# Optimization experiments

Measured on AMD Instinct MI355X. Metric: run time of the kernel, lower is better.

Reference implementation:

```python
import jax, jax.numpy as jnp
import numpy as np

B, N, DS, DP, H, DH, DFF = 1, 1024, 768, 128, 16, 48, 1536


def _ln(x, eps=1e-5):
    m = jnp.mean(x, axis=-1, keepdims=True)
    v = jnp.var(x, axis=-1, keepdims=True)
    return (x - m) * jax.lax.rsqrt(v + eps)


def _ada_ln(a, s, gw, gb, bw):
    # AF3-style adaptive layernorm: sigmoid(Linear(LN(s))) * LN(a) + Linear(LN(s))
    sn = _ln(s)
    return jax.nn.sigmoid(sn @ gw + gb) * _ln(a) + sn @ bw


def setup_inputs() -> dict:
    key = jax.random.key(0)
    ks = jax.random.split(key, 24)
    w = lambda k, shape: jax.random.normal(k, shape, dtype=jnp.float32) * 0.02
    return {
        'x': jax.random.normal(ks[0], (B, N, DS), dtype=jnp.float32),
        'single_cond': jax.random.normal(ks[1], (B, N, DS), dtype=jnp.float32),
        'pair_cond': jax.random.normal(ks[2], (B, N, N, DP), dtype=jnp.float32),
        'attn_gamma_w': w(ks[3], (DS, DS)), 'attn_gamma_b': jnp.zeros((DS,), jnp.float32),
        'attn_beta_w': w(ks[4], (DS, DS)),
        'wq': w(ks[5], (DS, H * DH)), 'bq': jnp.zeros((H * DH,), jnp.float32),
        'wk': w(ks[6], (DS, H * DH)), 'wv': w(ks[7], (DS, H * DH)),
        'wb': w(ks[8], (DP, H)),
        'wg': w(ks[9], (DS, H * DH)),
        'wo': w(ks[10], (H * DH, DS)),
        'attn_gate_w': w(ks[11], (DS, DS)), 'attn_gate_b': jnp.full((DS,), -2.0, jnp.float32),
        'ff_gamma_w': w(ks[12], (DS, DS)), 'ff_gamma_b': jnp.zeros((DS,), jnp.float32),
        'ff_beta_w': w(ks[13], (DS, DS)),
        'ff_w1': w(ks[14], (DS, DFF)), 'ff_w2': w(ks[15], (DS, DFF)),
        'ff_w3': w(ks[16], (DFF, DS)),
        'ff_gate_w': w(ks[17], (DS, DS)), 'ff_gate_b': jnp.full((DS,), -2.0, jnp.float32),
        'mask': jnp.ones((B, N), dtype=bool),
    }


def reference(x, single_cond, pair_cond, attn_gamma_w, attn_gamma_b, attn_beta_w,
              wq, bq, wk, wv, wb, wg, wo, attn_gate_w, attn_gate_b,
              ff_gamma_w, ff_gamma_b, ff_beta_w, ff_w1, ff_w2, ff_w3,
              ff_gate_w, ff_gate_b, mask):
    # --- AttentionPairBias (edge bias + cond adaLN + gated output) ---
    a = _ada_ln(x, single_cond, attn_gamma_w, attn_gamma_b, attn_beta_w)
    q = (a @ wq + bq).reshape(B, N, H, DH)  # q has bias (q_use_bias=True)
    k = (a @ wk).reshape(B, N, H, DH)
    v = (a @ wv).reshape(B, N, H, DH)
    bias = jnp.einsum('bijp,ph->bhij', _ln(pair_cond), wb)  # pair bias per head
    logits = jnp.einsum('bihd,bjhd->bhij', q, k) * (1.0 / np.float32(np.sqrt(DH))) + bias
    logits = jnp.where(mask[:, None, None, :], logits, jnp.float32(-1e9))
    attn = jax.nn.softmax(logits, axis=-1)
    o = jnp.einsum('bhij,bjhd->bihd', attn, v)
    g = jax.nn.sigmoid(a @ wg).reshape(B, N, H, DH)  # gating (g_use_bias=False)
    attn_out = (g * o).reshape(B, N, H * DH) @ wo  # o_use_bias=False
    attn_out = jax.nn.sigmoid(single_cond @ attn_gate_w + attn_gate_b) * attn_out
    # --- ConditionedFeedForward (adaLN + SwiGLU + cond output gate) ---
    f = _ada_ln(x, single_cond, ff_gamma_w, ff_gamma_b, ff_beta_w)
    h = jax.nn.silu(f @ ff_w1) * (f @ ff_w2)
    ff_out = jax.nn.sigmoid(single_cond @ ff_gate_w + ff_gate_b) * (h @ ff_w3)
    # dropout p=0 (eval) -> identity; residual add of both branches
    return x + attn_out + ff_out
```

## Files before the change

kernel.cpp:

```cpp
#include <hip/hip_runtime.h>
#include <hip/hip_bf16.h>


typedef __attribute__((ext_vector_type(8))) short bf16x8;
typedef __attribute__((ext_vector_type(4))) float f32x4;
typedef __attribute__((ext_vector_type(4))) unsigned short us4;

#define DEVFN static __device__ __forceinline__

DEVFN float bf2f(unsigned short u){
  union { unsigned int u; float f; } v; v.u = ((unsigned int)u) << 16; return v.f;
}
DEVFN unsigned short f2bf(float f){
  union { float f; unsigned int u; } v; v.f = f;
  unsigned int r = v.u + 0x7fffu + ((v.u >> 16) & 1u);
  return (unsigned short)(r >> 16);
}
DEVFN float sigf(float x){ return 1.f / (1.f + __expf(-x)); }

DEVFN void gload16(const void* g, void* l){
  __builtin_amdgcn_global_load_lds(
      (const __attribute__((address_space(1))) void*)g,
      (__attribute__((address_space(3))) void*)l, 16, 0, 0);
}

#define OFF_SN    0x0000000ULL
#define OFF_SC    0x0180000ULL
#define OFF_XA    0x0300000ULL
#define OFF_W1    0x0600000ULL
#define OFF_W2    0x0A80000ULL
#define OFF_W3    0x0CC0000ULL
#define OFF_W4    0x1140000ULL
#define OFF_W5    0x15C0000ULL
#define OFF_W6    0x1800000ULL
#define OFF_BIAS1 0x1920000ULL
#define OFF_BIASG 0x1923000ULL
#define OFF_BIASQ 0x1924800ULL
#define OFF_G1    0x1930000ULL
#define OFF_GATES 0x2530000ULL
#define OFF_A     0x2B30000ULL
#define OFF_F     0x2CB0000ULL
#define OFF_QKVG  0x2E30000ULL
#define OFF_VT    0x3430000ULL
#define OFF_HH    0x4030000ULL
#define OFF_GO    0x4330000ULL
#define OFF_PB    0x47B0000ULL

struct WJobs {
  const float* src[14];
  unsigned long long dst[14];
  int K[14];
  int N[14];
  int rowmul[14];
  int rowoff[14];
};

__global__ __launch_bounds__(256) void prep_kernel(WJobs jobs, char* ws,
    const float* __restrict__ x, const float* __restrict__ sc,
    unsigned short* __restrict__ sn_bf, unsigned short* __restrict__ sc_bf,
    float* __restrict__ xa,
    const float* agb, const float* bq, const float* gtb, const float* fgtb,
    const float* fgb, float* bias1, float* biasg, float* biasq){
  const int bid = blockIdx.x;
  const int tid = threadIdx.x;
  if(bid < 9792){
    int t = bid, z = 0;
    while(true){
      int nt = (jobs.N[z] >> 5) * (jobs.K[z] >> 5);
      if(t < nt) break;
      t -= nt; z++;
    }
    const int nx = jobs.N[z] >> 5;
    const int n0 = (t % nx) << 5, k0 = (t / nx) << 5;
    const int K = jobs.K[z], N = jobs.N[z];
    __shared__ float tt[32][33];
    const int tx = tid & 31, ty = tid >> 5;
    const float* src = jobs.src[z];
    #pragma unroll
    for(int i=0;i<4;i++)
      tt[ty + i*8][tx] = src[(long long)(k0 + ty + i*8) * N + n0 + tx];
    __syncthreads();
    unsigned short* dst = (unsigned short*)(ws + jobs.dst[z]);
    const int rm = jobs.rowmul[z], ro = jobs.rowoff[z];
    #pragma unroll
    for(int i=0;i<4;i++)
      dst[(long long)((n0 + ty + i*8)*rm + ro) * K + k0 + tx] = f2bf(tt[tx][ty + i*8]);
    return;
  }
  if(bid >= 10816){
    int t = (bid - 10816) * 256 + tid;
    float v = 0.f;
    if(t < 768) v = agb[t];
    else if(t >= 1536 && t < 2304) v = fgb[t - 1536];
    bias1[t] = v;
    biasq[t] = (t < 768) ? bq[t] : 0.f;
    if(t < 1536) biasg[t] = (t < 768) ? gtb[t] : fgtb[t - 768];
    return;
  }
  const int row = bid - 9792;
  const float* xr = x + (long long)row * 768;
  const float* sr = sc + (long long)row * 768;
  float xs[3], ss[3];
  float s0=0.f, s1=0.f, s2=0.f, s3=0.f;
  #pragma unroll
  for(int i=0;i<3;i++){
    float xv = xr[tid + i*256], sv = sr[tid + i*256];
    xs[i]=xv; ss[i]=sv;
    s0 += xv; s1 += xv*xv; s2 += sv; s3 += sv*sv;
  }
  #pragma unroll
  for(int o=32;o;o>>=1){
    s0 += __shfl_xor(s0,o); s1 += __shfl_xor(s1,o);
    s2 += __shfl_xor(s2,o); s3 += __shfl_xor(s3,o);
  }
  __shared__ float red[4][4];
  const int w = tid >> 6;
  if((tid & 63) == 0){ red[0][w]=s0; red[1][w]=s1; red[2][w]=s2; red[3][w]=s3; }
  __syncthreads();
  float tx0 = red[0][0]+red[0][1]+red[0][2]+red[0][3];
  float tx1 = red[1][0]+red[1][1]+red[1][2]+red[1][3];
  float ts0 = red[2][0]+red[2][1]+red[2][2]+red[2][3];
  float ts1 = red[3][0]+red[3][1]+red[3][2]+red[3][3];
  const float inv = 1.f/768.f;
  float mx = tx0*inv, vx = tx1*inv - mx*mx;
  float ms = ts0*inv, vs = ts1*inv - ms*ms;
  float rsx = rsqrtf(vx + 1e-5f), rss = rsqrtf(vs + 1e-5f);
  #pragma unroll
  for(int i=0;i<3;i++){
    int c = tid + i*256;
    xa[(long long)row*768 + c]    = (xs[i]-mx)*rsx;
    sn_bf[(long long)row*768 + c] = f2bf((ss[i]-ms)*rss);
    sc_bf[(long long)row*768 + c] = f2bf(ss[i]);
  }
}

DEVFN void gemm_tile_f32(const unsigned short* __restrict__ A,
                         const unsigned short* __restrict__ Bt,
                         int N, int K, int m0, int n0,
                         const float* __restrict__ bias,
                         float* __restrict__ Cf, int epi,
                         unsigned short* sA, unsigned short* sB, int tid){
  const int w = tid >> 6, l = tid & 63, l15 = l & 15, l4 = l >> 4;
  const int wm = w >> 1, wn = w & 1;
  f32x4 zf = {0.f,0.f,0.f,0.f};
  f32x4 acc[4][4];
  #pragma unroll
  for(int m=0;m<4;m++)
    #pragma unroll
    for(int n=0;n<4;n++) acc[m][n] = zf;

  const int srow = w*16 + (l >> 2);
  const int scol = (l & 3) * 8;
  const unsigned short* gA = A  + (long long)(m0 + srow) * K + scol;
  const unsigned short* gB = Bt + (long long)(n0 + srow) * K + scol;
  unsigned short* lA0 = &sA[(w*16)*32];
  unsigned short* lA1 = &sA[(64 + w*16)*32];
  unsigned short* lB0 = &sB[(w*16)*32];
  unsigned short* lB1 = &sB[(64 + w*16)*32];
  const long long half = (long long)64 * K;

  for(int k0 = 0; k0 < K; k0 += 32){
    gload16(gA + k0, lA0);
    gload16(gA + half + k0, lA1);
    gload16(gB + k0, lB0);
    gload16(gB + half + k0, lB1);
    __syncthreads();
    bf16x8 af[4], bg[4];
    #pragma unroll
    for(int m=0;m<4;m++) af[m] = *(const bf16x8*)&sA[(wm*64 + m*16 + l15)*32 + l4*8];
    #pragma unroll
    for(int n=0;n<4;n++) bg[n] = *(const bf16x8*)&sB[(wn*64 + n*16 + l15)*32 + l4*8];
    #pragma unroll
    for(int m=0;m<4;m++)
      #pragma unroll
      for(int n=0;n<4;n++)
        acc[m][n] = __builtin_amdgcn_mfma_f32_16x16x32_bf16(af[m], bg[n], acc[m][n], 0, 0, 0);
    __syncthreads();
  }
  #pragma unroll
  for(int m=0;m<4;m++){
    #pragma unroll
    for(int n=0;n<4;n++){
      #pragma unroll
      for(int r=0;r<4;r++){
        const int i = m0 + wm*64 + m*16 + l4*4 + r;
        const int c = n0 + wn*64 + n*16 + l15;
        float v = acc[m][n][r] + bias[c];
        Cf[(long long)i*N + c] = epi ? sigf(v) : v;
      }
    }
  }
}

DEVFN void pair_block(int pbid, const float* __restrict__ pair,
                      const float* __restrict__ wb,
                      unsigned short* __restrict__ pb, int tid){
  const int l = tid & 63, w = tid >> 6, l15 = l & 15, l4 = l >> 4;
  bf16x8 wbf[4];
  #pragma unroll
  for(int c=0;c<4;c++){
    bf16x8 t;
    #pragma unroll
    for(int e=0;e<8;e++) t[e] = (short)f2bf(wb[(c*32 + l4*8 + e)*16 + l15]);
    wbf[c] = t;
  }
  f32x4 zf = {0.f,0.f,0.f,0.f};
  #pragma unroll
  for(int q=0;q<4;q++){
    const long long tile = (long long)pbid * 16 + q*4 + w;
    const long long row0 = tile << 4;
    const float* pr = pair + ((row0 + l15) << 7);
    float vals[32];
    #pragma unroll
    for(int c=0;c<4;c++){
      float4 v0 = *(const float4*)(pr + c*32 + l4*8);
      float4 v1 = *(const float4*)(pr + c*32 + l4*8 + 4);
      vals[c*8+0]=v0.x; vals[c*8+1]=v0.y; vals[c*8+2]=v0.z; vals[c*8+3]=v0.w;
      vals[c*8+4]=v1.x; vals[c*8+5]=v1.y; vals[c*8+6]=v1.z; vals[c*8+7]=v1.w;
    }
    float s=0.f, s2=0.f;
    #pragma unroll
    for(int e=0;e<32;e++){ s += vals[e]; s2 += vals[e]*vals[e]; }
    s += __shfl_xor(s, 16); s2 += __shfl_xor(s2, 16);
    s += __shfl_xor(s, 32); s2 += __shfl_xor(s2, 32);
    const float m = s * (1.f/128.f);
    const float rs = rsqrtf(s2*(1.f/128.f) - m*m + 1e-5f);
    f32x4 acc = zf;
    #pragma unroll
    for(int c=0;c<4;c++){
      bf16x8 af;
      #pragma unroll
      for(int e=0;e<8;e++) af[e] = (short)f2bf((vals[c*8+e] - m) * rs);
      acc = __builtin_amdgcn_mfma_f32_16x16x32_bf16(af, wbf[c], acc, 0,0,0);
    }
    us4 o;
    #pragma unroll
    for(int r=0;r<4;r++) o[r] = f2bf(acc[r]);
    *(us4*)&pb[((long long)l15 << 20) + row0 + l4*4] = o;
  }
}

__global__ __launch_bounds__(256) void fA_kernel(
    const float* __restrict__ pair, const float* __restrict__ wb,
    unsigned short* __restrict__ pb,
    const unsigned short* __restrict__ SN, const unsigned short* __restrict__ W1,
    const float* __restrict__ B1, float* __restrict__ G1,
    const unsigned short* __restrict__ SC, const unsigned short* __restrict__ W2,
    const float* __restrict__ BG, float* __restrict__ GT){
  __shared__ unsigned short sA[128*32];
  __shared__ unsigned short sB[128*32];
  const int bid = blockIdx.x;
  const int tid = threadIdx.x;
  if(bid < 288){
    if(bid < 192){
      gemm_tile_f32(SN, W1, 3072, 768, (bid & 7)*128, (bid >> 3)*128, B1, G1, 0, sA, sB, tid);
    } else {
      const int t = bid - 192;
      gemm_tile_f32(SC, W2, 1536, 768, (t & 7)*128, (t >> 3)*128, BG, GT, 1, sA, sB, tid);
    }
    return;
  }
  pair_block(bid - 288, pair, wb, pb, tid);
}

__global__ __launch_bounds__(256) void ew1_kernel(const float* __restrict__ g1,
    const float* __restrict__ xa, unsigned short* __restrict__ a_bf,
    unsigned short* __restrict__ f_bf, const float* __restrict__ x,
    float* __restrict__ out){
  const int i = blockIdx.x;
  const int c = blockIdx.y * 256 + threadIdx.x;
  const float* row = g1 + (long long)i * 3072;
  float xv = xa[(long long)i*768 + c];
  a_bf[(long long)i*768 + c] = f2bf(sigf(row[c])      * xv + row[768 + c]);
  f_bf[(long long)i*768 + c] = f2bf(sigf(row[1536+c]) * xv + row[2304 + c]);
  out[(long long)i*768 + c] = x[(long long)i*768 + c];
}

__global__ __launch_bounds__(256) void fB_kernel(
    const float* __restrict__ pair, const float* __restrict__ wb,
    unsigned short* __restrict__ pb,
    const unsigned short* __restrict__ A_, const unsigned short* __restrict__ W3,
    const float* __restrict__ BQ, unsigned short* __restrict__ QKVG,
    unsigned short* __restrict__ VT,
    const unsigned short* __restrict__ F_, const unsigned short* __restrict__ W4,
    unsigned short* __restrict__ HH){
  __shared__ unsigned short sA[128*32];
  __shared__ unsigned short sB[128*32];
  const int bid = blockIdx.x;
  const int tid = threadIdx.x;
  if(bid >= 384){
    pair_block(bid - 384 + 2048, pair, wb, pb, tid);
    return;
  }
  const bool isq = bid < 192;
  const int t = isq ? bid : bid - 192;
  const int m0 = (t & 7) * 128, n0 = (t >> 3) * 128;
  const unsigned short* A  = isq ? A_ : F_;
  const unsigned short* Bt = isq ? W3 : W4;
  const int K = 768;

  const int w = tid >> 6, l = tid & 63, l15 = l & 15, l4 = l >> 4;
  const int wm = w >> 1, wn = w & 1;
  f32x4 zf = {0.f,0.f,0.f,0.f};
  f32x4 acc[4][4];
  #pragma unroll
  for(int m=0;m<4;m++)
    #pragma unroll
    for(int n=0;n<4;n++) acc[m][n] = zf;

  const int srow = w*16 + (l >> 2);
  const int scol = (l & 3) * 8;
  const unsigned short* gA = A  + (long long)(m0 + srow) * K + scol;
  const unsigned short* gB = Bt + (long long)(n0 + srow) * K + scol;
  unsigned short* lA0 = &sA[(w*16)*32];
  unsigned short* lA1 = &sA[(64 + w*16)*32];
  unsigned short* lB0 = &sB[(w*16)*32];
  unsigned short* lB1 = &sB[(64 + w*16)*32];
  const long long half = (long long)64 * K;

  for(int k0 = 0; k0 < K; k0 += 32){
    gload16(gA + k0, lA0);
    gload16(gA + half + k0, lA1);
    gload16(gB + k0, lB0);
    gload16(gB + half + k0, lB1);
    __syncthreads();
    bf16x8 af[4], bg[4];
    #pragma unroll
    for(int m=0;m<4;m++) af[m] = *(const bf16x8*)&sA[(wm*64 + m*16 + l15)*32 + l4*8];
    #pragma unroll
    for(int n=0;n<4;n++) bg[n] = *(const bf16x8*)&sB[(wn*64 + n*16 + l15)*32 + l4*8];
    #pragma unroll
    for(int m=0;m<4;m++)
      #pragma unroll
      for(int n=0;n<4;n++)
        acc[m][n] = __builtin_amdgcn_mfma_f32_16x16x32_bf16(af[m], bg[n], acc[m][n], 0, 0, 0);
    __syncthreads();
  }
  if(isq){
    #pragma unroll
    for(int m=0;m<4;m++){
      #pragma unroll
      for(int n=0;n<4;n++){
        const int c = n0 + wn*64 + n*16 + l15;
        const int ibase = m0 + wm*64 + m*16 + l4*4;
        unsigned short vb[4];
        #pragma unroll
        for(int r=0;r<4;r++){
          vb[r] = f2bf(acc[m][n][r] + BQ[c]);
          QKVG[(long long)(ibase + r)*3072 + c] = vb[r];
        }
        if(c >= 1536 && c < 2304){
          us4 o; o.x=vb[0]; o.y=vb[1]; o.z=vb[2]; o.w=vb[3];
          *(us4*)&VT[((long long)(c - 1536) << 10) + ibase] = o;
        }
      }
    }
  } else {
    #pragma unroll
    for(int m=0;m<4;m++){
      #pragma unroll
      for(int n=0;n<4;n++){
        #pragma unroll
        for(int r=0;r<4;r++){
          const int i = m0 + wm*64 + m*16 + l4*4 + r;
          const int c = n0 + wn*64 + n*16 + l15;
          float v = acc[m][n][r];
          float partner = __shfl_xor(v, 1);
          if((c & 1) == 0)
            HH[(long long)i*1536 + (c>>1)] = f2bf(v * sigf(v) * partner);
        }
      }
    }
  }
}

__global__ __launch_bounds__(256) void attn_kernel(
    const unsigned short* __restrict__ qkvg,
    const unsigned short* __restrict__ pbias,
    const unsigned short* __restrict__ VT,
    unsigned short* __restrict__ go){
  const int h  = blockIdx.x >> 6;
  const int i0 = (blockIdx.x & 63) << 4;
  const int tid = threadIdx.x;
  const int w = tid >> 6, l = tid & 63, l15 = l & 15, l4 = l >> 4;

  __shared__ unsigned short sP[16][1032];
  __shared__ float sRedM[16][4];
  __shared__ float sRedS[16][4];
  __shared__ float sO[4][16][48];

  f32x4 zf = {0.f,0.f,0.f,0.f};
  bf16x8 zero8 = {0,0,0,0,0,0,0,0};

  const unsigned short* pbh = pbias + ((long long)h << 20) + ((long long)i0 << 10);
  #pragma unroll
  for(int it=0; it<8; it++){
    const int idx = it*2048 + tid*8;
    const int r = idx >> 10, c = idx & 1023;
    *(bf16x8*)&sP[r][c] = *(const bf16x8*)&pbh[((long long)r << 10) + c];
  }

  f32x4 accs[16];
  #pragma unroll
  for(int f=0;f<16;f++) accs[f] = zf;
  bf16x8 aq0, aq1;
  {
    const unsigned short* qp = qkvg + (long long)(i0 + l15)*3072 + h*48;
    aq0 = *(const bf16x8*)(qp + l4*8);
    aq1 = *(const bf16x8*)(qp + 32 + l4*8);
  }
  const int jbase = w * 256;
  #pragma unroll
  for(int f=0; f<16; f++){
    const int j = jbase + f*16 + l15;
    const unsigned short* kp = qkvg + (long long)j*3072 + 768 + h*48;
    bf16x8 bk0 = *(const bf16x8*)(kp + l4*8);
    bf16x8 bk1 = *(const bf16x8*)(kp + 32 + l4*8);
    if(l4 >= 2) bk1 = zero8;
    accs[f] = __builtin_amdgcn_mfma_f32_16x16x32_bf16(aq0, bk0, accs[f], 0,0,0);
    accs[f] = __builtin_amdgcn_mfma_f32_16x16x32_bf16(aq1, bk1, accs[f], 0,0,0);
  }
  __syncthreads();

  const float scale = 0.14433756729740643f;
  #pragma unroll
  for(int f=0;f<16;f++){
    #pragma unroll
    for(int r=0;r<4;r++)
      accs[f][r] = accs[f][r]*scale + bf2f(sP[l4*4 + r][jbase + f*16 + l15]);
  }
  float pm[4];
  #pragma unroll
  for(int r=0;r<4;r++){
    float m = accs[0][r];
    #pragma unroll
    for(int f=1;f<16;f++) m = fmaxf(m, accs[f][r]);
    #pragma unroll
    for(int o=1;o<16;o<<=1) m = fmaxf(m, __shfl_xor(m, o));
    pm[r] = m;
  }
  if(l15 == 0){
    #pragma unroll
    for(int r=0;r<4;r++) sRedM[l4*4 + r][w] = pm[r];
  }
  __syncthreads();
  float rowm[4];
  #pragma unroll
  for(int r=0;r<4;r++){
    const int i = l4*4 + r;
    rowm[r] = fmaxf(fmaxf(sRedM[i][0], sRedM[i][1]), fmaxf(sRedM[i][2], sRedM[i][3]));
  }
  float psum[4] = {0.f,0.f,0.f,0.f};
  #pragma unroll
  for(int f=0;f<16;f++)
    #pragma unroll
    for(int r=0;r<4;r++){
      float p = __expf(accs[f][r] - rowm[r]);
      accs[f][r] = p;
      psum[r] += p;
    }
  #pragma unroll
  for(int r=0;r<4;r++)
    #pragma unroll
    for(int o=1;o<16;o<<=1) psum[r] += __shfl_xor(psum[r], o);
  if(l15 == 0){
    #pragma unroll
    for(int r=0;r<4;r++) sRedS[l4*4 + r][w] = psum[r];
  }
  #pragma unroll
  for(int f=0;f<16;f++)
    #pragma unroll
    for(int r=0;r<4;r++)
      sP[l4*4 + r][jbase + f*16 + l15] = f2bf(accs[f][r]);

  f32x4 acco[3];
  #pragma unroll
  for(int n=0;n<3;n++) acco[n] = zf;
  const unsigned short* vth = VT + ((long long)(h*48) << 10);
  #pragma unroll
  for(int c=0; c<4; c++){
    const int jb = jbase + c*64;
    #pragma unroll
    for(int kk=0; kk<2; kk++){
      bf16x8 pa = *(const bf16x8*)&sP[l15][jb + kk*32 + l4*8];
      #pragma unroll
      for(int n=0;n<3;n++){
        bf16x8 bv = *(const bf16x8*)&vth[((long long)(n*16 + l15) << 10) + jb + kk*32 + l4*8];
        acco[n] = __builtin_amdgcn_mfma_f32_16x16x32_bf16(pa, bv, acco[n], 0,0,0);
      }
    }
  }
  #pragma unroll
  for(int n=0;n<3;n++)
    #pragma unroll
    for(int r=0;r<4;r++)
      sO[w][l4*4 + r][n*16 + l15] = acco[n][r];
  __syncthreads();
  for(int t = tid; t < 768; t += 256){
    const int i = t / 48, d = t % 48;
    float o = sO[0][i][d] + sO[1][i][d] + sO[2][i][d] + sO[3][i][d];
    float lsum = sRedS[i][0] + sRedS[i][1] + sRedS[i][2] + sRedS[i][3];
    float gv = bf2f(qkvg[(long long)(i0 + i)*3072 + 2304 + h*48 + d]);
    go[(long long)(i0 + i)*768 + h*48 + d] = f2bf(sigf(gv) * (o / lsum));
  }
}

__global__ __launch_bounds__(256) void final_kernel(
    const unsigned short* __restrict__ GO, const unsigned short* __restrict__ W6t,
    const unsigned short* __restrict__ HH, const unsigned short* __restrict__ W5t,
    const float* __restrict__ gates, float* __restrict__ out){
  __shared__ unsigned short sA[128*32];
  __shared__ unsigned short sB[128*32];
  const int m0 = blockIdx.x * 128, n0 = blockIdx.y * 128;
  const int z = blockIdx.z;
  const bool pA = z < 4;
  const unsigned short* A  = pA ? GO  : HH;
  const unsigned short* Bt = pA ? W6t : W5t;
  const int K    = pA ? 768 : 1536;
  const int kbeg = pA ? z*192 : (z-4)*384;
  const int kend = pA ? kbeg + 192 : kbeg + 384;
  const int goff = pA ? 0 : 768;
  const int tid = threadIdx.x;
  const int w = tid >> 6, l = tid & 63, l15 = l & 15, l4 = l >> 4;
  const int wm = w >> 1, wn = w & 1;
  f32x4 zf = {0.f,0.f,0.f,0.f};
  f32x4 acc[4][4];
  #pragma unroll
  for(int m=0;m<4;m++)
    #pragma unroll
    for(int n=0;n<4;n++) acc[m][n] = zf;

  const int srow = w*16 + (l >> 2);
  const int scol = (l & 3) * 8;
  const unsigned short* gA = A  + (long long)(m0 + srow) * K + scol;
  const unsigned short* gB = Bt + (long long)(n0 + srow) * K + scol;
  unsigned short* lA0 = &sA[(w*16)*32];
  unsigned short* lA1 = &sA[(64 + w*16)*32];
  unsigned short* lB0 = &sB[(w*16)*32];
  unsigned short* lB1 = &sB[(64 + w*16)*32];
  const long long half = (long long)64 * K;

  for(int k0 = kbeg; k0 < kend; k0 += 32){
    gload16(gA + k0, lA0);
    gload16(gA + half + k0, lA1);
    gload16(gB + k0, lB0);
    gload16(gB + half + k0, lB1);
    __syncthreads();
    bf16x8 af[4], bg[4];
    #pragma unroll
    for(int m=0;m<4;m++) af[m] = *(const bf16x8*)&sA[(wm*64 + m*16 + l15)*32 + l4*8];
    #pragma unroll
    for(int n=0;n<4;n++) bg[n] = *(const bf16x8*)&sB[(wn*64 + n*16 + l15)*32 + l4*8];
    #pragma unroll
    for(int m=0;m<4;m++)
      #pragma unroll
      for(int n=0;n<4;n++)
        acc[m][n] = __builtin_amdgcn_mfma_f32_16x16x32_bf16(af[m], bg[n], acc[m][n], 0, 0, 0);
    __syncthreads();
  }
  #pragma unroll
  for(int m=0;m<4;m++){
    #pragma unroll
    for(int n=0;n<4;n++){
      #pragma unroll
      for(int r=0;r<4;r++){
        const int i = m0 + wm*64 + m*16 + l4*4 + r;
        const int c = n0 + wn*64 + n*16 + l15;
        float v = gates[(long long)i*1536 + goff + c] * acc[m][n][r];
        __hip_atomic_fetch_add(&out[(long long)i*768 + c], v,
                               __ATOMIC_RELAXED, __HIP_MEMORY_SCOPE_AGENT);
      }
    }
  }
}

extern "C" void kernel_launch(void* const* d_in, const int* in_sizes, int n_in,
                              void* d_out, int out_size, void* d_ws, size_t ws_size,
                              hipStream_t stream){
  (void)in_sizes; (void)n_in; (void)out_size; (void)ws_size;
  const float* x    = (const float*)d_in[0];
  const float* sc   = (const float*)d_in[1];
  const float* pair = (const float*)d_in[2];
  const float* agw  = (const float*)d_in[3];
  const float* agb  = (const float*)d_in[4];
  const float* abw  = (const float*)d_in[5];
  const float* wq   = (const float*)d_in[6];
  const float* bq   = (const float*)d_in[7];
  const float* wk   = (const float*)d_in[8];
  const float* wv   = (const float*)d_in[9];
  const float* wb   = (const float*)d_in[10];
  const float* wg   = (const float*)d_in[11];
  const float* wo   = (const float*)d_in[12];
  const float* gtw  = (const float*)d_in[13];
  const float* gtb  = (const float*)d_in[14];
  const float* fgw  = (const float*)d_in[15];
  const float* fgb  = (const float*)d_in[16];
  const float* fbw  = (const float*)d_in[17];
  const float* fw1  = (const float*)d_in[18];
  const float* fw2  = (const float*)d_in[19];
  const float* fw3  = (const float*)d_in[20];
  const float* fgtw = (const float*)d_in[21];
  const float* fgtb = (const float*)d_in[22];
  float* out = (float*)d_out;
  char* ws = (char*)d_ws;

  unsigned short* SN   = (unsigned short*)(ws + OFF_SN);
  unsigned short* SC   = (unsigned short*)(ws + OFF_SC);
  float*          XA   = (float*)(ws + OFF_XA);
  unsigned short* W1   = (unsigned short*)(ws + OFF_W1);
  unsigned short* W2   = (unsigned short*)(ws + OFF_W2);
  unsigned short* W3   = (unsigned short*)(ws + OFF_W3);
  unsigned short* W4   = (unsigned short*)(ws + OFF_W4);
  unsigned short* W5   = (unsigned short*)(ws + OFF_W5);
  unsigned short* W6   = (unsigned short*)(ws + OFF_W6);
  float*          B1   = (float*)(ws + OFF_BIAS1);
  float*          BG   = (float*)(ws + OFF_BIASG);
  float*          BQ   = (float*)(ws + OFF_BIASQ);
  float*          G1   = (float*)(ws + OFF_G1);
  float*          GT   = (float*)(ws + OFF_GATES);
  unsigned short* A_   = (unsigned short*)(ws + OFF_A);
  unsigned short* F_   = (unsigned short*)(ws + OFF_F);
  unsigned short* QKVG = (unsigned short*)(ws + OFF_QKVG);
  unsigned short* VT   = (unsigned short*)(ws + OFF_VT);
  unsigned short* HH   = (unsigned short*)(ws + OFF_HH);
  unsigned short* GO   = (unsigned short*)(ws + OFF_GO);
  unsigned short* PB   = (unsigned short*)(ws + OFF_PB);

  WJobs jobs;
  int ji = 0;
  auto setj = [&](const float* s, unsigned long long off, int K, int N,
                  int rm = 1, int ro = 0){
    jobs.src[ji]=s; jobs.dst[ji]=off; jobs.K[ji]=K; jobs.N[ji]=N;
    jobs.rowmul[ji]=rm; jobs.rowoff[ji]=ro; ji++;
  };
  const unsigned long long W768 = 768ULL*768ULL*2ULL;
  setj(agw,  OFF_W1 + 0*W768, 768, 768);
  setj(abw,  OFF_W1 + 1*W768, 768, 768);
  setj(fgw,  OFF_W1 + 2*W768, 768, 768);
  setj(fbw,  OFF_W1 + 3*W768, 768, 768);
  setj(gtw,  OFF_W2 + 0*W768, 768, 768);
  setj(fgtw, OFF_W2 + 1*W768, 768, 768);
  setj(wq,   OFF_W3 + 0*W768, 768, 768);
  setj(wk,   OFF_W3 + 1*W768, 768, 768);
  setj(wv,   OFF_W3 + 2*W768, 768, 768);
  setj(wg,   OFF_W3 + 3*W768, 768, 768);
  setj(fw1,  OFF_W4, 768, 1536, 2, 0);
  setj(fw2,  OFF_W4, 768, 1536, 2, 1);
  setj(fw3,  OFF_W5, 1536, 768);
  setj(wo,   OFF_W6, 768, 768);

  prep_kernel<<<10828, 256, 0, stream>>>(jobs, ws, x, sc, SN, SC, XA,
      agb, bq, gtb, fgtb, fgb, B1, BG, BQ);
  fA_kernel<<<2336, 256, 0, stream>>>(pair, wb, PB, SN, W1, B1, G1, SC, W2, BG, GT);
  ew1_kernel<<<dim3(1024,3), 256, 0, stream>>>(G1, XA, A_, F_, x, out);
  fB_kernel<<<2432, 256, 0, stream>>>(pair, wb, PB, A_, W3, BQ, QKVG, VT, F_, W4, HH);
  attn_kernel<<<1024, 256, 0, stream>>>(QKVG, PB, VT, GO);
  final_kernel<<<dim3(8,6,8), 256, 0, stream>>>(GO, W6, HH, W5, GT, out);
}
```

Baseline: 273.7 us.

## Defer weight transposes into fA, interleave GEMM and pair blocks, fuse final residual

The weight transpose jobs not needed by the first GEMMs move out of prep_kernel and into fA_kernel, where they run alongside the pair-bias blocks. GEMM tiles in fA and fB are spread across the grid (every 30th or 6th block) so they overlap with the memory-bound pair work rather than all running first. final_kernel is rewritten to use 64x64 tiles that do the full K reduction for both branches and write x plus the gated sums directly. This removes the atomics and the separate out=x copy in ew1_kernel. The cost is fewer, longer final blocks (192 in total) with a serial K loop, and more complex block index mapping.

```diff
diff --git a/kernel.cpp b/kernel.cpp
--- a/kernel.cpp
+++ b/kernel.cpp
@@ -47,13 +47,38 @@
 #define OFF_PB    0x47B0000ULL
 
 struct WJobs {
-  const float* src[14];
-  unsigned long long dst[14];
-  int K[14];
-  int N[14];
-  int rowmul[14];
-  int rowoff[14];
+  const float* src[8];
+  unsigned long long dst[8];
+  int K[8];
+  int N[8];
+  int rowmul[8];
+  int rowoff[8];
+  int njobs;
 };
+
+DEVFN void transpose_tile(const WJobs& jobs, char* ws, int t, int tid, void* smem){
+  int z = 0;
+  while(true){
+    int nt = (jobs.N[z] >> 5) * (jobs.K[z] >> 5);
+    if(t < nt) break;
+    t -= nt; z++;
+  }
+  const int nx = jobs.N[z] >> 5;
+  const int n0 = (t % nx) << 5, k0 = (t / nx) << 5;
+  const int K = jobs.K[z], N = jobs.N[z];
+  float (*tt)[33] = (float(*)[33])smem;
+  const int tx = tid & 31, ty = tid >> 5;
+  const float* src = jobs.src[z];
+  #pragma unroll
+  for(int i=0;i<4;i++)
+    tt[ty + i*8][tx] = src[(long long)(k0 + ty + i*8) * N + n0 + tx];
+  __syncthreads();
+  unsigned short* dst = (unsigned short*)(ws + jobs.dst[z]);
+  const int rm = jobs.rowmul[z], ro = jobs.rowoff[z];
+  #pragma unroll
+  for(int i=0;i<4;i++)
+    dst[(long long)((n0 + ty + i*8)*rm + ro) * K + k0 + tx] = f2bf(tt[tx][ty + i*8]);
+}
 
 __global__ __launch_bounds__(256) void prep_kernel(WJobs jobs, char* ws,
     const float* __restrict__ x, const float* __restrict__ sc,
@@ -61,34 +86,15 @@
     float* __restrict__ xa,
     const float* agb, const float* bq, const float* gtb, const float* fgtb,
     const float* fgb, float* bias1, float* biasg, float* biasq){
+  __shared__ __align__(16) char smem[4352];
   const int bid = blockIdx.x;
   const int tid = threadIdx.x;
-  if(bid < 9792){
-    int t = bid, z = 0;
-    while(true){
-      int nt = (jobs.N[z] >> 5) * (jobs.K[z] >> 5);
-      if(t < nt) break;
-      t -= nt; z++;
-    }
-    const int nx = jobs.N[z] >> 5;
-    const int n0 = (t % nx) << 5, k0 = (t / nx) << 5;
-    const int K = jobs.K[z], N = jobs.N[z];
-    __shared__ float tt[32][33];
-    const int tx = tid & 31, ty = tid >> 5;
-    const float* src = jobs.src[z];
-    #pragma unroll
-    for(int i=0;i<4;i++)
-      tt[ty + i*8][tx] = src[(long long)(k0 + ty + i*8) * N + n0 + tx];
-    __syncthreads();
-    unsigned short* dst = (unsigned short*)(ws + jobs.dst[z]);
-    const int rm = jobs.rowmul[z], ro = jobs.rowoff[z];
-    #pragma unroll
-    for(int i=0;i<4;i++)
-      dst[(long long)((n0 + ty + i*8)*rm + ro) * K + k0 + tx] = f2bf(tt[tx][ty + i*8]);
+  if(bid < 3456){
+    transpose_tile(jobs, ws, bid, tid, smem);
     return;
   }
-  if(bid >= 10816){
-    int t = (bid - 10816) * 256 + tid;
+  if(bid >= 4480){
+    int t = (bid - 4480) * 256 + tid;
     float v = 0.f;
     if(t < 768) v = agb[t];
     else if(t >= 1536 && t < 2304) v = fgb[t - 1536];
@@ -97,7 +103,7 @@
     if(t < 1536) biasg[t] = (t < 768) ? gtb[t] : fgtb[t - 768];
     return;
   }
-  const int row = bid - 9792;
+  const int row = bid - 3456;
   const float* xr = x + (long long)row * 768;
   const float* sr = sc + (long long)row * 768;
   float xs[3], ss[3];
@@ -113,7 +119,7 @@
     s0 += __shfl_xor(s0,o); s1 += __shfl_xor(s1,o);
     s2 += __shfl_xor(s2,o); s3 += __shfl_xor(s3,o);
   }
-  __shared__ float red[4][4];
+  float (*red)[4] = (float(*)[4])smem;
   const int w = tid >> 6;
   if((tid & 63) == 0){ red[0][w]=s0; red[1][w]=s1; red[2][w]=s2; red[3][w]=s3; }
   __syncthreads();
@@ -241,39 +247,44 @@
 }
 
 __global__ __launch_bounds__(256) void fA_kernel(
+    WJobs jobsA, char* ws,
     const float* __restrict__ pair, const float* __restrict__ wb,
     unsigned short* __restrict__ pb,
     const unsigned short* __restrict__ SN, const unsigned short* __restrict__ W1,
     const float* __restrict__ B1, float* __restrict__ G1,
     const unsigned short* __restrict__ SC, const unsigned short* __restrict__ W2,
     const float* __restrict__ BG, float* __restrict__ GT){
-  __shared__ unsigned short sA[128*32];
-  __shared__ unsigned short sB[128*32];
+  __shared__ __align__(16) unsigned short sA[128*32];
+  __shared__ __align__(16) unsigned short sB[128*32];
   const int bid = blockIdx.x;
   const int tid = threadIdx.x;
-  if(bid < 288){
-    if(bid < 192){
-      gemm_tile_f32(SN, W1, 3072, 768, (bid & 7)*128, (bid >> 3)*128, B1, G1, 0, sA, sB, tid);
+  const int g30 = bid / 30;
+  if((bid % 30) == 0 && g30 < 288){
+    if(g30 < 192){
+      gemm_tile_f32(SN, W1, 3072, 768, (g30 & 7)*128, (g30 >> 3)*128, B1, G1, 0, sA, sB, tid);
     } else {
-      const int t = bid - 192;
+      const int t = g30 - 192;
       gemm_tile_f32(SC, W2, 1536, 768, (t & 7)*128, (t >> 3)*128, BG, GT, 1, sA, sB, tid);
     }
     return;
   }
-  pair_block(bid - 288, pair, wb, pb, tid);
+  const int rid = bid - (((bid % 30) == 0) ? 288 : min(g30 + 1, 288));
+  if(rid < 6336){
+    transpose_tile(jobsA, ws, rid, tid, sA);
+    return;
+  }
+  pair_block(rid - 6336, pair, wb, pb, tid);
 }
 
 __global__ __launch_bounds__(256) void ew1_kernel(const float* __restrict__ g1,
     const float* __restrict__ xa, unsigned short* __restrict__ a_bf,
-    unsigned short* __restrict__ f_bf, const float* __restrict__ x,
-    float* __restrict__ out){
+    unsigned short* __restrict__ f_bf){
   const int i = blockIdx.x;
   const int c = blockIdx.y * 256 + threadIdx.x;
   const float* row = g1 + (long long)i * 3072;
   float xv = xa[(long long)i*768 + c];
   a_bf[(long long)i*768 + c] = f2bf(sigf(row[c])      * xv + row[768 + c]);
   f_bf[(long long)i*768 + c] = f2bf(sigf(row[1536+c]) * xv + row[2304 + c]);
-  out[(long long)i*768 + c] = x[(long long)i*768 + c];
 }
 
 __global__ __launch_bounds__(256) void fB_kernel(
@@ -284,16 +295,18 @@
     unsigned short* __restrict__ VT,
     const unsigned short* __restrict__ F_, const unsigned short* __restrict__ W4,
     unsigned short* __restrict__ HH){
-  __shared__ unsigned short sA[128*32];
-  __shared__ unsigned short sB[128*32];
+  __shared__ __align__(16) unsigned short sA[128*32];
+  __shared__ __align__(16) unsigned short sB[128*32];
   const int bid = blockIdx.x;
   const int tid = threadIdx.x;
-  if(bid >= 384){
-    pair_block(bid - 384 + 2048, pair, wb, pb, tid);
+  const int g6 = bid / 6;
+  if((bid % 6) != 0 || g6 >= 384){
+    const int rid = bid - (((bid % 6) == 0) ? 384 : min(g6 + 1, 384));
+    pair_block(rid + 2048, pair, wb, pb, tid);
     return;
   }
-  const bool isq = bid < 192;
-  const int t = isq ? bid : bid - 192;
+  const bool isq = g6 < 192;
+  const int t = isq ? g6 : g6 - 192;
   const int m0 = (t & 7) * 128, n0 = (t >> 3) * 128;
   const unsigned short* A  = isq ? A_ : F_;
   const unsigned short* Bt = isq ? W3 : W4;
@@ -508,67 +521,82 @@
 __global__ __launch_bounds__(256) void final_kernel(
     const unsigned short* __restrict__ GO, const unsigned short* __restrict__ W6t,
     const unsigned short* __restrict__ HH, const unsigned short* __restrict__ W5t,
-    const float* __restrict__ gates, float* __restrict__ out){
-  __shared__ unsigned short sA[128*32];
-  __shared__ unsigned short sB[128*32];
-  const int m0 = blockIdx.x * 128, n0 = blockIdx.y * 128;
-  const int z = blockIdx.z;
-  const bool pA = z < 4;
-  const unsigned short* A  = pA ? GO  : HH;
-  const unsigned short* Bt = pA ? W6t : W5t;
-  const int K    = pA ? 768 : 1536;
-  const int kbeg = pA ? z*192 : (z-4)*384;
-  const int kend = pA ? kbeg + 192 : kbeg + 384;
-  const int goff = pA ? 0 : 768;
+    const float* __restrict__ gates, const float* __restrict__ x,
+    float* __restrict__ out){
+  __shared__ __align__(16) unsigned short sA[64*32];
+  __shared__ __align__(16) unsigned short sB[64*32];
+  const int m0 = (blockIdx.x >> 4) * 64, n0 = (blockIdx.x & 15) * 48;
+  const int mi = blockIdx.x / 12, ni = blockIdx.x % 12;
+  const int M0 = mi * 64, N0 = ni * 64;
+  (void)m0; (void)n0;
   const int tid = threadIdx.x;
   const int w = tid >> 6, l = tid & 63, l15 = l & 15, l4 = l >> 4;
   const int wm = w >> 1, wn = w & 1;
   f32x4 zf = {0.f,0.f,0.f,0.f};
-  f32x4 acc[4][4];
-  #pragma unroll
-  for(int m=0;m<4;m++)
-    #pragma unroll
-    for(int n=0;n<4;n++) acc[m][n] = zf;
-
-  const int srow = w*16 + (l >> 2);
-  const int scol = (l & 3) * 8;
-  const unsigned short* gA = A  + (long long)(m0 + srow) * K + scol;
-  const unsigned short* gB = Bt + (long long)(n0 + srow) * K + scol;
-  unsigned short* lA0 = &sA[(w*16)*32];
-  unsigned short* lA1 = &sA[(64 + w*16)*32];
-  unsigned short* lB0 = &sB[(w*16)*32];
-  unsigned short* lB1 = &sB[(64 + w*16)*32];
-  const long long half = (long long)64 * K;
-
-  for(int k0 = kbeg; k0 < kend; k0 += 32){
-    gload16(gA + k0, lA0);
-    gload16(gA + half + k0, lA1);
-    gload16(gB + k0, lB0);
-    gload16(gB + half + k0, lB1);
-    __syncthreads();
-    bf16x8 af[4], bg[4];
-    #pragma unroll
-    for(int m=0;m<4;m++) af[m] = *(const bf16x8*)&sA[(wm*64 + m*16 + l15)*32 + l4*8];
-    #pragma unroll
-    for(int n=0;n<4;n++) bg[n] = *(const bf16x8*)&sB[(wn*64 + n*16 + l15)*32 + l4*8];
-    #pragma unroll
-    for(int m=0;m<4;m++)
-      #pragma unroll
-      for(int n=0;n<4;n++)
-        acc[m][n] = __builtin_amdgcn_mfma_f32_16x16x32_bf16(af[m], bg[n], acc[m][n], 0, 0, 0);
-    __syncthreads();
-  }
-  #pragma unroll
-  for(int m=0;m<4;m++){
-    #pragma unroll
-    for(int n=0;n<4;n++){
+  f32x4 accA[2][2], accB[2][2];
+  #pragma unroll
+  for(int m=0;m<2;m++)
+    #pragma unroll
+    for(int n=0;n<2;n++){ accA[m][n] = zf; accB[m][n] = zf; }
+
+  const int srow = tid >> 2;
+  const int scol = (tid & 3) * 8;
+  unsigned short* lA = &sA[w*16*32];
+  unsigned short* lB = &sB[w*16*32];
+
+  {
+    const int K = 768;
+    const unsigned short* gA = GO  + (long long)(M0 + srow) * K + scol;
+    const unsigned short* gB = W6t + (long long)(N0 + srow) * K + scol;
+    for(int k0 = 0; k0 < K; k0 += 32){
+      gload16(gA + k0, lA);
+      gload16(gB + k0, lB);
+      __syncthreads();
+      bf16x8 af[2], bg[2];
+      #pragma unroll
+      for(int m=0;m<2;m++) af[m] = *(const bf16x8*)&sA[(wm*32 + m*16 + l15)*32 + l4*8];
+      #pragma unroll
+      for(int n=0;n<2;n++) bg[n] = *(const bf16x8*)&sB[(wn*32 + n*16 + l15)*32 + l4*8];
+      #pragma unroll
+      for(int m=0;m<2;m++)
+        #pragma unroll
+        for(int n=0;n<2;n++)
+          accA[m][n] = __builtin_amdgcn_mfma_f32_16x16x32_bf16(af[m], bg[n], accA[m][n], 0, 0, 0);
+      __syncthreads();
+    }
+  }
+  {
+    const int K = 1536;
+    const unsigned short* gA = HH  + (long long)(M0 + srow) * K + scol;
+    const unsigned short* gB = W5t + (long long)(N0 + srow) * K + scol;
+    for(int k0 = 0; k0 < K; k0 += 32){
+      gload16(gA + k0, lA);
+      gload16(gB + k0, lB);
+      __syncthreads();
+      bf16x8 af[2], bg[2];
+      #pragma unroll
+      for(int m=0;m<2;m++) af[m] = *(const bf16x8*)&sA[(wm*32 + m*16 + l15)*32 + l4*8];
+      #pragma unroll
+      for(int n=0;n<2;n++) bg[n] = *(const bf16x8*)&sB[(wn*32 + n*16 + l15)*32 + l4*8];
+      #pragma unroll
+      for(int m=0;m<2;m++)
+        #pragma unroll
+        for(int n=0;n<2;n++)
+          accB[m][n] = __builtin_amdgcn_mfma_f32_16x16x32_bf16(af[m], bg[n], accB[m][n], 0, 0, 0);
+      __syncthreads();
+    }
+  }
+  #pragma unroll
+  for(int m=0;m<2;m++){
+    #pragma unroll
+    for(int n=0;n<2;n++){
       #pragma unroll
       for(int r=0;r<4;r++){
-        const int i = m0 + wm*64 + m*16 + l4*4 + r;
-        const int c = n0 + wn*64 + n*16 + l15;
-        float v = gates[(long long)i*1536 + goff + c] * acc[m][n][r];
-        __hip_atomic_fetch_add(&out[(long long)i*768 + c], v,
-                               __ATOMIC_RELAXED, __HIP_MEMORY_SCOPE_AGENT);
+        const int i = M0 + wm*32 + m*16 + l4*4 + r;
+        const int c = N0 + wn*32 + n*16 + l15;
+        out[(long long)i*768 + c] = x[(long long)i*768 + c]
+            + gates[(long long)i*1536 + c]       * accA[m][n][r]
+            + gates[(long long)i*1536 + 768 + c] * accB[m][n][r];
       }
     }
   }
@@ -626,34 +654,47 @@
   unsigned short* GO   = (unsigned short*)(ws + OFF_GO);
   unsigned short* PB   = (unsigned short*)(ws + OFF_PB);
 
-  WJobs jobs;
-  int ji = 0;
-  auto setj = [&](const float* s, unsigned long long off, int K, int N,
-                  int rm = 1, int ro = 0){
-    jobs.src[ji]=s; jobs.dst[ji]=off; jobs.K[ji]=K; jobs.N[ji]=N;
-    jobs.rowmul[ji]=rm; jobs.rowoff[ji]=ro; ji++;
-  };
   const unsigned long long W768 = 768ULL*768ULL*2ULL;
-  setj(agw,  OFF_W1 + 0*W768, 768, 768);
-  setj(abw,  OFF_W1 + 1*W768, 768, 768);
-  setj(fgw,  OFF_W1 + 2*W768, 768, 768);
-  setj(fbw,  OFF_W1 + 3*W768, 768, 768);
-  setj(gtw,  OFF_W2 + 0*W768, 768, 768);
-  setj(fgtw, OFF_W2 + 1*W768, 768, 768);
-  setj(wq,   OFF_W3 + 0*W768, 768, 768);
-  setj(wk,   OFF_W3 + 1*W768, 768, 768);
-  setj(wv,   OFF_W3 + 2*W768, 768, 768);
-  setj(wg,   OFF_W3 + 3*W768, 768, 768);
-  setj(fw1,  OFF_W4, 768, 1536, 2, 0);
-  setj(fw2,  OFF_W4, 768, 1536, 2, 1);
-  setj(fw3,  OFF_W5, 1536, 768);
-  setj(wo,   OFF_W6, 768, 768);
-
-  prep_kernel<<<10828, 256, 0, stream>>>(jobs, ws, x, sc, SN, SC, XA,
+
+  WJobs jobsP; jobsP.njobs = 6;
+  {
+    int ji = 0;
+    auto setj = [&](const float* s, unsigned long long off, int K, int N,
+                    int rm, int ro){
+      jobsP.src[ji]=s; jobsP.dst[ji]=off; jobsP.K[ji]=K; jobsP.N[ji]=N;
+      jobsP.rowmul[ji]=rm; jobsP.rowoff[ji]=ro; ji++;
+    };
+    setj(agw,  OFF_W1 + 0*W768, 768, 768, 1, 0);
+    setj(abw,  OFF_W1 + 1*W768, 768, 768, 1, 0);
+    setj(fgw,  OFF_W1 + 2*W768, 768, 768, 1, 0);
+    setj(fbw,  OFF_W1 + 3*W768, 768, 768, 1, 0);
+    setj(gtw,  OFF_W2 + 0*W768, 768, 768, 1, 0);
+    setj(fgtw, OFF_W2 + 1*W768, 768, 768, 1, 0);
+  }
+  WJobs jobsA; jobsA.njobs = 8;
+  {
+    int ji = 0;
+    auto setj = [&](const float* s, unsigned long long off, int K, int N,
+                    int rm, int ro){
+      jobsA.src[ji]=s; jobsA.dst[ji]=off; jobsA.K[ji]=K; jobsA.N[ji]=N;
+      jobsA.rowmul[ji]=rm; jobsA.rowoff[ji]=ro; ji++;
+    };
+    setj(wq,   OFF_W3 + 0*W768, 768, 768, 1, 0);
+    setj(wk,   OFF_W3 + 1*W768, 768, 768, 1, 0);
+    setj(wv,   OFF_W3 + 2*W768, 768, 768, 1, 0);
+    setj(wg,   OFF_W3 + 3*W768, 768, 768, 1, 0);
+    setj(fw1,  OFF_W4, 768, 1536, 2, 0);
+    setj(fw2,  OFF_W4, 768, 1536, 2, 1);
+    setj(fw3,  OFF_W5, 1536, 768, 1, 0);
+    setj(wo,   OFF_W6, 768, 768, 1, 0);
+  }
+
+  prep_kernel<<<4492, 256, 0, stream>>>(jobsP, ws, x, sc, SN, SC, XA,
       agb, bq, gtb, fgtb, fgb, B1, BG, BQ);
-  fA_kernel<<<2336, 256, 0, stream>>>(pair, wb, PB, SN, W1, B1, G1, SC, W2, BG, GT);
-  ew1_kernel<<<dim3(1024,3), 256, 0, stream>>>(G1, XA, A_, F_, x, out);
+  fA_kernel<<<8672, 256, 0, stream>>>(jobsA, ws, pair, wb, PB,
+      SN, W1, B1, G1, SC, W2, BG, GT);
+  ew1_kernel<<<dim3(1024,3), 256, 0, stream>>>(G1, XA, A_, F_);
   fB_kernel<<<2432, 256, 0, stream>>>(pair, wb, PB, A_, W3, BQ, QKVG, VT, F_, W4, HH);
   attn_kernel<<<1024, 256, 0, stream>>>(QKVG, PB, VT, GO);
-  final_kernel<<<dim3(8,6,8), 256, 0, stream>>>(GO, W6, HH, W5, GT, out);
-}
+  final_kernel<<<192, 256, 0, stream>>>(GO, W6, HH, W5, GT, x, out);
+}
```

Result: slower. 296.4 us (+8.3%).
